# Kernel tuning notes

Measured on AMD Instinct MI355X. Metric: run time of the kernel, lower is better.

## Reference

```python
import jax, jax.numpy as jnp
import numpy as np

NUM_HEADS = 16
ROPE_BASE = 10000.0


def rotate_half(x):
    d = x.shape[-1] // 2
    return jnp.concatenate([-x[..., d:], x[..., :d]], axis=-1)


def setup_inputs() -> dict:
    key = jax.random.key(0)
    ks = jax.random.split(key, 6)
    B, S, H = 2, 2048, 1024
    scale = 1.0 / np.sqrt(H)  # ~xavier for square matrices
    x = jax.random.normal(ks[0], (B, S, H), dtype=jnp.float32)
    Wq = jax.random.normal(ks[1], (H, H), dtype=jnp.float32) * scale
    Wk = jax.random.normal(ks[2], (H, H), dtype=jnp.float32) * scale
    Wv = jax.random.normal(ks[3], (H, H), dtype=jnp.float32) * scale
    Wo = jax.random.normal(ks[4], (H, H), dtype=jnp.float32) * scale
    # learnable bias, tril-initialized as in the torch module
    bias = jnp.tril(jax.random.normal(ks[5], (S, S), dtype=jnp.float32) * 0.02)
    return {"x": x, "Wq": Wq, "Wk": Wk, "Wv": Wv, "Wo": Wo, "bias": bias}


def reference(x, Wq, Wk, Wv, Wo, bias):
    B, S, H = x.shape
    nh = NUM_HEADS
    hd = H // nh

    # projections (torch Linear: y = x @ W.T), split heads -> [B, nh, S, hd]
    q = (x @ Wq.T).reshape(B, S, nh, hd).transpose(0, 2, 1, 3)
    k = (x @ Wk.T).reshape(B, S, nh, hd).transpose(0, 2, 1, 3)
    v = (x @ Wv.T).reshape(B, S, nh, hd).transpose(0, 2, 1, 3)

    # rotary embeddings, position_ids = arange(S)
    inv_freq = 1.0 / (ROPE_BASE ** (jnp.arange(0, hd, 2, dtype=jnp.float32) / hd))
    t = jnp.arange(S, dtype=jnp.float32)
    freqs = t[:, None] * inv_freq[None, :]          # [S, hd/2]
    emb = jnp.concatenate([freqs, freqs], axis=-1)  # [S, hd]
    cos = jnp.cos(emb).astype(x.dtype)
    sin = jnp.sin(emb).astype(x.dtype)
    q = q * cos + rotate_half(q) * sin
    k = k * cos + rotate_half(k) * sin

    # scores + learnable bias + causal mask
    scores = jnp.einsum('bhqd,bhkd->bhqk', q, k) / np.float32(np.sqrt(hd))
    scores = scores + bias[:S, :S][None, None, :, :]
    causal = jnp.tril(jnp.ones((S, S), dtype=bool))
    scores = jnp.where(causal, scores, -jnp.inf)

    attn = jax.nn.softmax(scores, axis=-1)
    out = jnp.einsum('bhqk,bhkd->bhqd', attn, v)
    out = out.transpose(0, 2, 1, 3).reshape(B, S, H)
    return out @ Wo.T, attn
```

## Files before the change

kernel.cpp:

```cpp
#include <hip/hip_runtime.h>
#include <hip/hip_bf16.h>
#include <math.h>


typedef __attribute__((ext_vector_type(8))) short bx8;
typedef __attribute__((ext_vector_type(4))) short sx4;
typedef __attribute__((ext_vector_type(4))) float fx4;
typedef __attribute__((ext_vector_type(4))) float f4v;

#define MFMA_BF16(a, b, c) __builtin_amdgcn_mfma_f32_16x16x32_bf16(a, b, c, 0, 0, 0)
#define LOG2E 1.44269504088896340736f

__device__ __forceinline__ short f2bf(float f) {
    union { float f; unsigned u; } v; v.f = f;
    unsigned u = v.u;
    u += 0x7fffu + ((u >> 16) & 1u);
    return (short)(u >> 16);
}
__device__ __forceinline__ float u2f(unsigned u) {
    union { unsigned u; float f; } v; v.u = u; return v.f;
}
__device__ __forceinline__ float bf2f(short s) {
    return u2f(((unsigned)(unsigned short)s) << 16);
}

__device__ __forceinline__ bx8 pack8(f4v a, f4v b) {
    bx8 r;
    r[0] = f2bf(a[0]); r[1] = f2bf(a[1]); r[2] = f2bf(a[2]); r[3] = f2bf(a[3]);
    r[4] = f2bf(b[0]); r[5] = f2bf(b[1]); r[6] = f2bf(b[2]); r[7] = f2bf(b[3]);
    return r;
}

__device__ __forceinline__ void gload_lds16(const short* g, short* l) {
    __builtin_amdgcn_global_load_lds(
        (const __attribute__((address_space(1))) void*)g,
        (__attribute__((address_space(3))) void*)l, 16, 0, 0);
}

__global__ __launch_bounds__(256) void cast_kernel(
        const float* __restrict__ x, const float* __restrict__ Wq,
        const float* __restrict__ Wk, const float* __restrict__ Wv,
        const float* __restrict__ Wo, const float* __restrict__ bias,
        short* __restrict__ dst, short* __restrict__ bias_bf)
{
    const size_t M1 = 1u << 20;
    if (blockIdx.x < 4096) {
        const size_t e0 = ((size_t)blockIdx.x * 256 + threadIdx.x) * 8;
        const float* src; size_t off;
        if (e0 < 4 * M1) { src = x; off = e0; }
        else {
            const int j = (int)((e0 - 4 * M1) >> 20);
            src = (j == 0) ? Wq : (j == 1) ? Wk : (j == 2) ? Wv : Wo;
            off = (e0 - 4 * M1) & (M1 - 1);
        }
        f4v a = *(const f4v*)(src + off);
        f4v b = *(const f4v*)(src + off + 4);
        *(bx8*)(dst + e0) = pack8(a, b);
    } else {
        const size_t e0 = ((size_t)(blockIdx.x - 4096) * 256 + threadIdx.x) * 8;
        f4v a = *(const f4v*)(bias + e0);
        f4v b = *(const f4v*)(bias + e0 + 4);
        #pragma unroll
        for (int i = 0; i < 4; ++i) { a[i] *= LOG2E; b[i] *= LOG2E; }
        *(bx8*)(bias_bf + e0) = pack8(a, b);
    }
}

__global__ void rope_table_kernel(float* __restrict__ cosT, float* __restrict__ sinT) {
    int i = blockIdx.x * 256 + threadIdx.x;
    if (i >= 2048 * 64) return;
    int s = i >> 6, d = i & 63;
    int fi = d & 31;
    float inv_freq = powf(10000.0f, -(float)fi / 32.0f);
    float ang = (float)s * inv_freq;
    cosT[i] = cosf(ang);
    sinT[i] = sinf(ang);
}

template<int OUTPROJ>
__global__ __launch_bounds__(256) void gemm128(
        const short* __restrict__ A, const short* __restrict__ W0,
        const short* __restrict__ W1, const short* __restrict__ W2,
        const float* __restrict__ cosT, const float* __restrict__ sinT,
        void* __restrict__ Out)
{
    __shared__ short As[128][64];
    __shared__ short Bs[128][64];
    const int bm = blockIdx.x, bn = blockIdx.y, z = blockIdx.z;
    const short* W = OUTPROJ ? W0 : (z == 0 ? W0 : (z == 1 ? W1 : W2));
    const int tid = threadIdx.x, w = tid >> 6, lane = tid & 63;
    const int cl = lane & 15, lg = lane >> 4;
    const int srow = lane >> 3;
    const int schunk = (lane & 7) ^ srow;

    fx4 acc[4][4];
    #pragma unroll
    for (int mi = 0; mi < 4; ++mi)
        #pragma unroll
        for (int ni = 0; ni < 4; ++ni) acc[mi][ni] = (fx4){0.f, 0.f, 0.f, 0.f};

    const int wr = (w >> 1) * 64, wc = (w & 1) * 64;

    for (int k0 = 0; k0 < 1024; k0 += 64) {
        __syncthreads();
        #pragma unroll
        for (int i = 0; i < 4; ++i) {
            const int rbase = w * 32 + i * 8;
            gload_lds16(A + (size_t)(bm * 128 + rbase + srow) * 1024 + k0 + schunk * 8,
                        &As[rbase][0]);
            gload_lds16(W + (size_t)(bn * 128 + rbase + srow) * 1024 + k0 + schunk * 8,
                        &Bs[rbase][0]);
        }
        __syncthreads();
        #pragma unroll
        for (int kk = 0; kk < 2; ++kk) {
            bx8 af[4], bf[4];
            #pragma unroll
            for (int i = 0; i < 4; ++i) {
                const int ra = wr + i * 16 + cl;
                af[i] = *(const bx8*)&As[ra][((kk * 4 + lg) ^ (ra & 7)) * 8];
                const int rb = wc + i * 16 + cl;
                bf[i] = *(const bx8*)&Bs[rb][((kk * 4 + lg) ^ (rb & 7)) * 8];
            }
            #pragma unroll
            for (int mi = 0; mi < 4; ++mi)
                #pragma unroll
                for (int ni = 0; ni < 4; ++ni)
                    acc[mi][ni] = MFMA_BF16(af[mi], bf[ni], acc[mi][ni]);
        }
    }

    #pragma unroll
    for (int mi = 0; mi < 4; ++mi) {
        #pragma unroll
        for (int reg = 0; reg < 4; ++reg) {
            const int r = bm * 128 + wr + mi * 16 + (lg << 2) + reg;
            if constexpr (OUTPROJ) {
                #pragma unroll
                for (int ni = 0; ni < 4; ++ni) {
                    const int col = bn * 128 + wc + ni * 16 + cl;
                    ((float*)Out)[(size_t)r * 1024 + col] = acc[mi][ni][reg];
                }
            } else {
                const int b = r >> 11, s = r & 2047;
                const int h = bn * 2 + (wc >> 6);
                short* dst = (short*)Out + (size_t)z * 32 * 2048 * 64
                           + (size_t)((b * 16 + h) * 2048 + s) * 64;
                #pragma unroll
                for (int ni = 0; ni < 4; ++ni) {
                    const int d = ni * 16 + cl;
                    float v = acc[mi][ni][reg];
                    if (z <= 1) {
                        const float cs = cosT[s * 64 + d], sn = sinT[s * 64 + d];
                        const float partner = acc[mi][ni ^ 2][reg];
                        const float rot = (d < 32) ? -partner : partner;
                        v = v * cs + rot * sn;
                        if (z == 0) v *= 0.125f * LOG2E;
                    }
                    dst[d] = f2bf(v);
                }
            }
        }
    }
}

__global__ __launch_bounds__(256, 3) void attn_kernel(
        const short* __restrict__ Q, const short* __restrict__ K,
        const short* __restrict__ V, const short* __restrict__ bias_bf,
        float* __restrict__ attn_out, short* __restrict__ o_buf)
{
    const int S = 2048;
    const int bid = blockIdx.x;
    const int xcd = bid & 7, rr_ = bid >> 3;
    const int bh = xcd * 4 + (rr_ & 3);
    const int qt = 31 - (rr_ >> 2);
    const int h = bh & 15, b = bh >> 4;
    const int tid = threadIdx.x, w = tid >> 6, lane = tid & 63;
    const int cl = lane & 15, lg = lane >> 4;
    const size_t base = (size_t)bh * S * 64;
    const int NT = qt + 1;

    __shared__ short Ks[2][64][64];
    __shared__ short Vt[2][64][72];
    __shared__ short P[4][16][136];

    const int krow8 = lane >> 3, kchk = (lane & 7) ^ krow8;
    const int vrow = tid >> 2, vd0 = (tid & 3) * 16;

    const short* qp = Q + base + (size_t)(qt * 64 + w * 16 + cl) * 64 + lg * 8;
    const bx8 qf0 = *(const bx8*)qp;
    const bx8 qf1 = *(const bx8*)(qp + 32);
    const int qr  = qt * 64 + w * 16 + cl;
    const int sq0 = qt * 64 + w * 16 + (lg << 2);
    const short* brow = bias_bf + (size_t)qr * 2048;
    const size_t strip_base = ((size_t)bh * S + qt * 64 + w * 16) * S;

#define STAGEK(BUF, t)                                                            \
    { gload_lds16(K + base + (size_t)((t) * 64 + w * 16 + krow8) * 64 + kchk * 8, \
                  &Ks[BUF][w * 16][0]);                                           \
      gload_lds16(K + base + (size_t)((t) * 64 + w * 16 + 8 + krow8) * 64 + kchk * 8, \
                  &Ks[BUF][w * 16 + 8][0]); }

#define LOADB(BR, t)                                                              \
    { _Pragma("unroll") for (int n = 0; n < 4; ++n)                               \
        BR[n] = *(const sx4*)(brow + (t) * 64 + n * 16 + (lg << 2)); }

#define QKT(BUF, SACC)                                                            \
    { const int cs_ = cl & 7;                                                     \
      const fx4 zf = (fx4){0.f, 0.f, 0.f, 0.f};                                   \
      _Pragma("unroll") for (int n = 0; n < 4; ++n) {                             \
        bx8 a0 = *(const bx8*)&Ks[BUF][n * 16 + cl][(lg ^ cs_) * 8];              \
        bx8 a1 = *(const bx8*)&Ks[BUF][n * 16 + cl][((4 + lg) ^ cs_) * 8];        \
        SACC[n] = MFMA_BF16(a0, qf0, zf);                                         \
        SACC[n] = MFMA_BF16(a1, qf1, SACC[n]); } }

#define COMP_A(BUF, BR, t)                                                        \
    { fx4 sacc[4]; QKT(BUF, sacc);                                                \
      _Pragma("unroll") for (int n = 0; n < 4; ++n)                               \
        _Pragma("unroll") for (int e = 0; e < 4; ++e) {                           \
          const int kc = (t) * 64 + n * 16 + (lg << 2) + e;                       \
          const float sv = sacc[n][e] + bf2f(BR[n][e]);                           \
          lsum[n] += (kc <= qr) ? exp2f(sv) : 0.f; } }

#define LOADVr(V0, V1, t)                                                         \
    { const short* vp = V + base + (size_t)((t) * 64 + vrow) * 64 + vd0;          \
      V0 = *(const bx8*)vp; V1 = *(const bx8*)(vp + 8); }

#define VSTORE(V0, V1, BUF)                                                       \
    { _Pragma("unroll") for (int j = 0; j < 8; ++j) Vt[BUF][vd0 + j][vrow] = V0[j]; \
      _Pragma("unroll") for (int j = 0; j < 8; ++j) Vt[BUF][vd0 + 8 + j][vrow] = V1[j]; }

#define COMP_B(KBUF, BR, VBUF, t)                                                 \
    { fx4 sacc[4]; QKT(KBUF, sacc);                                               \
      _Pragma("unroll") for (int n = 0; n < 4; ++n) {                             \
        sx4 pb;                                                                   \
        _Pragma("unroll") for (int e = 0; e < 4; ++e) {                           \
          const int kc = (t) * 64 + n * 16 + (lg << 2) + e;                       \
          const float sv = sacc[n][e] + bf2f(BR[n][e]);                           \
          const float p = (kc <= qr) ? exp2f(sv - L2) : 0.f;                      \
          pb[e] = f2bf(p); }                                                      \
        *(sx4*)&P[w][cl][((t) & 1) * 64 + n * 16 + (lg << 2)] = pb; }             \
      _Pragma("unroll") for (int kk = 0; kk < 2; ++kk) {                          \
        bx8 pa = *(const bx8*)&P[w][cl][((t) & 1) * 64 + kk * 32 + lg * 8];       \
        _Pragma("unroll") for (int n = 0; n < 4; ++n) {                           \
          bx8 vb = *(const bx8*)&Vt[VBUF][n * 16 + cl][kk * 32 + lg * 8];         \
          oacc[n] = MFMA_BF16(pa, vb, oacc[n]); } } }

#define FLUSH2(tp)                                                                \
    { _Pragma("unroll") for (int rp = 0; rp < 16; rp += 2) {                      \
        const int row = rp + (lane >> 5), col = (lane & 31) * 4;                  \
        const unsigned* ps = (const unsigned*)&P[w][row][col];                    \
        const unsigned px = ps[0], py = ps[1];                                    \
        f4v o; o[0] = u2f(px << 16); o[1] = u2f(px & 0xffff0000u);                \
        o[2] = u2f(py << 16); o[3] = u2f(py & 0xffff0000u);                       \
        __builtin_nontemporal_store(o,                                            \
            (f4v*)(attn_out + strip_base + (size_t)row * S + (tp) * 64 + col)); } }

#define FLUSH1(tp)                                                                \
    { _Pragma("unroll") for (int rp = 0; rp < 16; rp += 4) {                      \
        const int row = rp + (lane >> 4), col = (lane & 15) * 4;                  \
        const unsigned* ps = (const unsigned*)&P[w][row][col];                    \
        const unsigned px = ps[0], py = ps[1];                                    \
        f4v o; o[0] = u2f(px << 16); o[1] = u2f(px & 0xffff0000u);                \
        o[2] = u2f(py << 16); o[3] = u2f(py & 0xffff0000u);                       \
        __builtin_nontemporal_store(o,                                            \
            (f4v*)(attn_out + strip_base + (size_t)row * S + (tp) * 64 + col)); } }

    float lsum[4] = {0.f, 0.f, 0.f, 0.f};

    {
        sx4 bA[4], bB[4];
        STAGEK(0, 0); LOADB(bA, 0);
        __syncthreads();
        int t = 0;
        for (; t + 1 < NT; t += 2) {
            STAGEK(1, t + 1); LOADB(bB, t + 1);
            COMP_A(0, bA, t);
            __syncthreads();
            if (t + 2 < NT) { STAGEK(0, t + 2); LOADB(bA, t + 2); }
            COMP_A(1, bB, t + 1);
            __syncthreads();
        }
        if (t < NT) COMP_A(0, bA, t);
    }

    float l = (lsum[0] + lsum[1]) + (lsum[2] + lsum[3]);
    l += __shfl_xor(l, 16);
    l += __shfl_xor(l, 32);
    const float L2 = __log2f(l);

    fx4 oacc[4];
    #pragma unroll
    for (int n = 0; n < 4; n++) oacc[n] = (fx4){0.f, 0.f, 0.f, 0.f};

    sx4 bA[4], bB[4];
    bx8 vA0, vA1, vB0, vB1;
    __syncthreads();
    STAGEK(0, 0); LOADB(bA, 0); LOADVr(vA0, vA1, 0);
    __syncthreads();
    VSTORE(vA0, vA1, 0);
    __syncthreads();
    int t = 0;
    for (; t + 1 < NT; t += 2) {
        STAGEK(1, t + 1); LOADB(bB, t + 1); LOADVr(vB0, vB1, t + 1);
        COMP_B(0, bA, 0, t);
        VSTORE(vB0, vB1, 1);
        __syncthreads();
        if (t + 2 < NT) { STAGEK(0, t + 2); LOADB(bA, t + 2); LOADVr(vA0, vA1, t + 2); }
        COMP_B(1, bB, 1, t + 1);
        FLUSH2(t);
        if (t + 2 < NT) VSTORE(vA0, vA1, 0);
        __syncthreads();
    }
    if (t < NT) { COMP_B(0, bA, 0, t); FLUSH1(t); }

    #pragma unroll
    for (int reg = 0; reg < 4; reg++) {
        const int sq = sq0 + reg;
        #pragma unroll
        for (int n = 0; n < 4; n++) {
            const int d = n * 16 + cl;
            o_buf[(size_t)(b * 2048 + sq) * 1024 + h * 64 + d] = f2bf(oacc[n][reg]);
        }
    }

    const int c0 = (qt + 1) * 64;
    if (c0 < S) {
        const f4v z = (f4v){0.f, 0.f, 0.f, 0.f};
        for (int r = w; r < 64; r += 4) {
            float* dst = attn_out + ((size_t)bh * S + qt * 64 + r) * S;
            for (int cc = c0 + lane * 4; cc < S; cc += 256)
                __builtin_nontemporal_store(z, (f4v*)(dst + cc));
        }
    }
#undef STAGEK
#undef LOADB
#undef QKT
#undef COMP_A
#undef LOADVr
#undef VSTORE
#undef COMP_B
#undef FLUSH2
#undef FLUSH1
}

extern "C" void kernel_launch(void* const* d_in, const int* in_sizes, int n_in,
                              void* d_out, int out_size, void* d_ws, size_t ws_size,
                              hipStream_t stream) {
    const float* x    = (const float*)d_in[0];
    const float* Wq   = (const float*)d_in[1];
    const float* Wk   = (const float*)d_in[2];
    const float* Wv   = (const float*)d_in[3];
    const float* Wo   = (const float*)d_in[4];
    const float* bias = (const float*)d_in[5];

    float* out  = (float*)d_out;
    float* attn = out + (size_t)2 * 2048 * 1024;

    char* ws = (char*)d_ws;
    const size_t M1 = 1u << 20;
    short* x_bf    = (short*)ws;
    short* wq_bf   = x_bf + 4 * M1;
    short* wk_bf   = wq_bf + M1;
    short* wv_bf   = wk_bf + M1;
    short* wo_bf   = wv_bf + M1;
    short* bias_bf = wo_bf + M1;
    float* cosT    = (float*)(ws + 24 * M1);
    float* sinT    = cosT + 2048 * 64;
    short* q_rope  = (short*)(ws + 25 * M1);
    short* k_rope  = q_rope + 4 * M1;
    short* v_bf    = k_rope + 4 * M1;
    short* o_buf   = x_bf;

    cast_kernel<<<6144, 256, 0, stream>>>(x, Wq, Wk, Wv, Wo, bias, x_bf, bias_bf);
    rope_table_kernel<<<512, 256, 0, stream>>>(cosT, sinT);
    gemm128<0><<<dim3(32, 8, 3), 256, 0, stream>>>(x_bf, wq_bf, wk_bf, wv_bf,
                                                   cosT, sinT, q_rope);
    attn_kernel<<<1024, 256, 0, stream>>>(q_rope, k_rope, v_bf, bias_bf, attn, o_buf);
    gemm128<1><<<dim3(32, 8, 1), 256, 0, stream>>>(o_buf, wo_bf, wo_bf, wo_bf,
                                                   cosT, sinT, out);
}
```

Before: 258.8 us.

## Double attention query tile to 128 rows with 512-thread blocks

Each attention block now handles 128 query rows with 8 waves instead of 64 rows with 4 waves, and the grid shrinks from 1024 to 512 blocks. K and V tiles staged in shared memory are reused by twice as many query rows, halving global K/V/transposed-V staging per query. Because NT is now always even, the odd-tile tail paths are removed. In exchange the causal work per block is less balanced, occupancy limits change, and the diagonal tiles waste more masked work.

After: 252.6 us. 1.02x faster.

```diff
diff --git a/kernel.cpp b/kernel.cpp
--- a/kernel.cpp
+++ b/kernel.cpp
@@ -164,7 +164,7 @@
     }
 }
 
-__global__ __launch_bounds__(256, 3) void attn_kernel(
+__global__ __launch_bounds__(512, 4) void attn_kernel(
         const short* __restrict__ Q, const short* __restrict__ K,
         const short* __restrict__ V, const short* __restrict__ bias_bf,
         float* __restrict__ attn_out, short* __restrict__ o_buf)
@@ -173,33 +173,31 @@
     const int bid = blockIdx.x;
     const int xcd = bid & 7, rr_ = bid >> 3;
     const int bh = xcd * 4 + (rr_ & 3);
-    const int qt = 31 - (rr_ >> 2);
+    const int qt = 15 - (rr_ >> 2);
     const int h = bh & 15, b = bh >> 4;
     const int tid = threadIdx.x, w = tid >> 6, lane = tid & 63;
     const int cl = lane & 15, lg = lane >> 4;
     const size_t base = (size_t)bh * S * 64;
-    const int NT = qt + 1;
+    const int NT = 2 * qt + 2;
 
     __shared__ short Ks[2][64][64];
     __shared__ short Vt[2][64][72];
-    __shared__ short P[4][16][136];
+    __shared__ short P[8][16][136];
 
     const int krow8 = lane >> 3, kchk = (lane & 7) ^ krow8;
-    const int vrow = tid >> 2, vd0 = (tid & 3) * 16;
-
-    const short* qp = Q + base + (size_t)(qt * 64 + w * 16 + cl) * 64 + lg * 8;
+    const int vrow = tid >> 3, vd0 = (tid & 7) * 8;
+
+    const short* qp = Q + base + (size_t)(qt * 128 + w * 16 + cl) * 64 + lg * 8;
     const bx8 qf0 = *(const bx8*)qp;
     const bx8 qf1 = *(const bx8*)(qp + 32);
-    const int qr  = qt * 64 + w * 16 + cl;
-    const int sq0 = qt * 64 + w * 16 + (lg << 2);
+    const int qr  = qt * 128 + w * 16 + cl;
+    const int sq0 = qt * 128 + w * 16 + (lg << 2);
     const short* brow = bias_bf + (size_t)qr * 2048;
-    const size_t strip_base = ((size_t)bh * S + qt * 64 + w * 16) * S;
+    const size_t strip_base = ((size_t)bh * S + qt * 128 + w * 16) * S;
 
 #define STAGEK(BUF, t)                                                            \
-    { gload_lds16(K + base + (size_t)((t) * 64 + w * 16 + krow8) * 64 + kchk * 8, \
-                  &Ks[BUF][w * 16][0]);                                           \
-      gload_lds16(K + base + (size_t)((t) * 64 + w * 16 + 8 + krow8) * 64 + kchk * 8, \
-                  &Ks[BUF][w * 16 + 8][0]); }
+    gload_lds16(K + base + (size_t)((t) * 64 + w * 8 + krow8) * 64 + kchk * 8,    \
+                &Ks[BUF][w * 8][0]);
 
 #define LOADB(BR, t)                                                              \
     { _Pragma("unroll") for (int n = 0; n < 4; ++n)                               \
@@ -222,13 +220,11 @@
           const float sv = sacc[n][e] + bf2f(BR[n][e]);                           \
           lsum[n] += (kc <= qr) ? exp2f(sv) : 0.f; } }
 
-#define LOADVr(V0, V1, t)                                                         \
-    { const short* vp = V + base + (size_t)((t) * 64 + vrow) * 64 + vd0;          \
-      V0 = *(const bx8*)vp; V1 = *(const bx8*)(vp + 8); }
-
-#define VSTORE(V0, V1, BUF)                                                       \
-    { _Pragma("unroll") for (int j = 0; j < 8; ++j) Vt[BUF][vd0 + j][vrow] = V0[j]; \
-      _Pragma("unroll") for (int j = 0; j < 8; ++j) Vt[BUF][vd0 + 8 + j][vrow] = V1[j]; }
+#define LOADVr(V0, t)                                                             \
+    V0 = *(const bx8*)(V + base + (size_t)((t) * 64 + vrow) * 64 + vd0);
+
+#define VSTORE(V0, BUF)                                                           \
+    { _Pragma("unroll") for (int j = 0; j < 8; ++j) Vt[BUF][vd0 + j][vrow] = V0[j]; }
 
 #define COMP_B(KBUF, BR, VBUF, t)                                                 \
     { fx4 sacc[4]; QKT(KBUF, sacc);                                               \
@@ -256,24 +252,13 @@
         __builtin_nontemporal_store(o,                                            \
             (f4v*)(attn_out + strip_base + (size_t)row * S + (tp) * 64 + col)); } }
 
-#define FLUSH1(tp)                                                                \
-    { _Pragma("unroll") for (int rp = 0; rp < 16; rp += 4) {                      \
-        const int row = rp + (lane >> 4), col = (lane & 15) * 4;                  \
-        const unsigned* ps = (const unsigned*)&P[w][row][col];                    \
-        const unsigned px = ps[0], py = ps[1];                                    \
-        f4v o; o[0] = u2f(px << 16); o[1] = u2f(px & 0xffff0000u);                \
-        o[2] = u2f(py << 16); o[3] = u2f(py & 0xffff0000u);                       \
-        __builtin_nontemporal_store(o,                                            \
-            (f4v*)(attn_out + strip_base + (size_t)row * S + (tp) * 64 + col)); } }
-
     float lsum[4] = {0.f, 0.f, 0.f, 0.f};
 
     {
         sx4 bA[4], bB[4];
         STAGEK(0, 0); LOADB(bA, 0);
         __syncthreads();
-        int t = 0;
-        for (; t + 1 < NT; t += 2) {
+        for (int t = 0; t + 1 < NT; t += 2) {
             STAGEK(1, t + 1); LOADB(bB, t + 1);
             COMP_A(0, bA, t);
             __syncthreads();
@@ -281,7 +266,6 @@
             COMP_A(1, bB, t + 1);
             __syncthreads();
         }
-        if (t < NT) COMP_A(0, bA, t);
     }
 
     float l = (lsum[0] + lsum[1]) + (lsum[2] + lsum[3]);
@@ -294,25 +278,22 @@
     for (int n = 0; n < 4; n++) oacc[n] = (fx4){0.f, 0.f, 0.f, 0.f};
 
     sx4 bA[4], bB[4];
-    bx8 vA0, vA1, vB0, vB1;
+    bx8 vA0, vB0;
+    STAGEK(0, 0); LOADB(bA, 0); LOADVr(vA0, 0);
     __syncthreads();
-    STAGEK(0, 0); LOADB(bA, 0); LOADVr(vA0, vA1, 0);
+    VSTORE(vA0, 0);
     __syncthreads();
-    VSTORE(vA0, vA1, 0);
-    __syncthreads();
-    int t = 0;
-    for (; t + 1 < NT; t += 2) {
-        STAGEK(1, t + 1); LOADB(bB, t + 1); LOADVr(vB0, vB1, t + 1);
+    for (int t = 0; t + 1 < NT; t += 2) {
+        STAGEK(1, t + 1); LOADB(bB, t + 1); LOADVr(vB0, t + 1);
         COMP_B(0, bA, 0, t);
-        VSTORE(vB0, vB1, 1);
-        __syncthreads();
-        if (t + 2 < NT) { STAGEK(0, t + 2); LOADB(bA, t + 2); LOADVr(vA0, vA1, t + 2); }
+        VSTORE(vB0, 1);
+        __syncthreads();
+        if (t + 2 < NT) { STAGEK(0, t + 2); LOADB(bA, t + 2); LOADVr(vA0, t + 2); }
         COMP_B(1, bB, 1, t + 1);
         FLUSH2(t);
-        if (t + 2 < NT) VSTORE(vA0, vA1, 0);
-        __syncthreads();
-    }
-    if (t < NT) { COMP_B(0, bA, 0, t); FLUSH1(t); }
+        if (t + 2 < NT) VSTORE(vA0, 0);
+        __syncthreads();
+    }
 
     #pragma unroll
     for (int reg = 0; reg < 4; reg++) {
@@ -324,11 +305,11 @@
         }
     }
 
-    const int c0 = (qt + 1) * 64;
+    const int c0 = (qt + 1) * 128;
     if (c0 < S) {
         const f4v z = (f4v){0.f, 0.f, 0.f, 0.f};
-        for (int r = w; r < 64; r += 4) {
-            float* dst = attn_out + ((size_t)bh * S + qt * 64 + r) * S;
+        for (int r = w; r < 128; r += 8) {
+            float* dst = attn_out + ((size_t)bh * S + qt * 128 + r) * S;
             for (int cc = c0 + lane * 4; cc < S; cc += 256)
                 __builtin_nontemporal_store(z, (f4v*)(dst + cc));
         }
@@ -341,7 +322,6 @@
 #undef VSTORE
 #undef COMP_B
 #undef FLUSH2
-#undef FLUSH1
 }
 
 extern "C" void kernel_launch(void* const* d_in, const int* in_sizes, int n_in,
@@ -376,7 +356,7 @@
     rope_table_kernel<<<512, 256, 0, stream>>>(cosT, sinT);
     gemm128<0><<<dim3(32, 8, 3), 256, 0, stream>>>(x_bf, wq_bf, wk_bf, wv_bf,
                                                    cosT, sinT, q_rope);
-    attn_kernel<<<1024, 256, 0, stream>>>(q_rope, k_rope, v_bf, bias_bf, attn, o_buf);
+    attn_kernel<<<512, 512, 0, stream>>>(q_rope, k_rope, v_bf, bias_bf, attn, o_buf);
     gemm128<1><<<dim3(32, 8, 1), 256, 0, stream>>>(o_buf, wo_bf, wo_bf, wo_bf,
                                                    cosT, sinT, out);
 }
```
